# Kernel tuning notes

Hardware: AMD Instinct MI355X
Metric: run time of the kernel (lower is better)

Reference implementation:

```python
import jax, jax.numpy as jnp
import numpy as np

NC = 32          # number of cells
NDIM = 1         # 1D CPAB
NSTEPS = 32      # nstepsolver


def _expm_affine1d(A):
    """Closed-form matrix exponential of [[a, b], [0, 0]] (batched).

    A: [M, 1, 2] -> returns [M, 2, 2] with expm = [[e^a, b*phi(a)], [0, 1]],
    phi(a) = (e^a - 1)/a, with a stable small-a branch.
    """
    a = A[:, 0, 0]
    b = A[:, 0, 1]
    small = jnp.abs(a) < 1e-6
    a_safe = jnp.where(small, 1.0, a)
    phi = jnp.where(small, 1.0 + 0.5 * a, jnp.expm1(a_safe) / a_safe)
    top = jnp.stack([jnp.exp(a), b * phi], axis=-1)            # [M, 2]
    bot = jnp.broadcast_to(jnp.array([0.0, 1.0], dtype=A.dtype), top.shape)
    return jnp.stack([top, bot], axis=-2)                       # [M, 2, 2]


def setup_inputs() -> dict:
    key = jax.random.key(0)
    k1, k2, k3 = jax.random.split(key, 3)
    n_points, n_theta, d = 262144, 8, 30
    points = jax.random.uniform(k1, (NDIM, n_points), dtype=jnp.float32)
    theta = 0.5 * jax.random.normal(k2, (n_theta, d), dtype=jnp.float32)
    basis = 0.3 * jax.random.normal(k3, ((NDIM + 1) * NDIM * NC, d), dtype=jnp.float32)
    return {"points": points, "theta": theta, "basis": basis}


def reference(points, theta, basis):
    n_points = points.shape[1]
    n_theta = theta.shape[0]
    dT = 1.0 / NSTEPS

    # Per-cell affine velocity matrices: Avees [2*nC, n_theta] -> As [n_theta*nC, 1, 2]
    Avees = basis @ theta.T
    As = Avees.T.reshape(n_theta * NC, NDIM, NDIM + 1)
    Trels = _expm_affine1d(dT * As)                               # [n_theta*nC, 2, 2]

    # Repeat points per theta (theta-major flatten order, matching torch code)
    x = jnp.tile(points[0], n_theta)                              # [N]
    pts = jnp.stack([x, jnp.ones_like(x)], axis=-1)               # [N, 2] homogeneous
    batch_idx = NC * jnp.repeat(jnp.arange(n_theta, dtype=jnp.int32), n_points)

    def step(p, _):
        cell = jnp.clip(jnp.floor(p[:, 0] * NC), 0, NC - 1).astype(jnp.int32)
        T = Trels[cell + batch_idx]                               # [N, 2, 2] gather
        return jnp.einsum('nij,nj->ni', T, p), None

    pts, _ = jax.lax.scan(step, pts, None, length=NSTEPS)

    # [N, 1] -> [n_theta, ndim, n_points]
    return pts[:, :NDIM].reshape(n_theta, n_points, NDIM).transpose(0, 2, 1)
```

## Files before the change

kernel.cpp:

```cpp
#include <hip/hip_runtime.h>
#include <math.h>

#define NC 32
#define NSTEPS 32

constexpr int BLOCK = 256;
constexpr int PTS_PER_THREAD = 4;
constexpr int CHUNK = BLOCK * PTS_PER_THREAD;

__global__ void __launch_bounds__(BLOCK)
cpab_kernel(const float* __restrict__ points,
            const float* __restrict__ theta,
            const float* __restrict__ basis,
            float* __restrict__ out,
            int n_points, int d) {
    __shared__ float2 tab[NC];

    const int blocks_per_theta = n_points / CHUNK;
    const int j = blockIdx.x / blocks_per_theta;
    const int tid = threadIdx.x;

    if (tid < NC) {
        const int c = tid;
        const float* __restrict__ th = theta + j * d;
        const float* __restrict__ ba = basis + (2 * c) * d;
        const float* __restrict__ bb = basis + (2 * c + 1) * d;
        float a = 0.0f, b = 0.0f;
#pragma unroll 6
        for (int k = 0; k < d; ++k) {
            float t = th[k];
            a = fmaf(ba[k], t, a);
            b = fmaf(bb[k], t, b);
        }
        const float dT = 1.0f / (float)NSTEPS;
        a *= dT;
        b *= dT;
        float A = expf(a);
        float phi = (fabsf(a) < 1e-6f) ? (1.0f + 0.5f * a) : (expm1f(a) / a);
        tab[c] = make_float2(A, b * phi);
    }
    __syncthreads();

    const int base = (blockIdx.x % blocks_per_theta) * CHUNK + tid * 4;

    float4 v = *(const float4*)(points + base);
    float x[PTS_PER_THREAD] = {v.x, v.y, v.z, v.w};

#pragma unroll
    for (int s = 0; s < NSTEPS; ++s) {
#pragma unroll
        for (int i = 0; i < PTS_PER_THREAD; ++i) {
            float cf = fminf(fmaxf(floorf(x[i] * (float)NC), 0.0f),
                             (float)(NC - 1));
            float2 t = tab[(int)cf];
            x[i] = fmaf(t.x, x[i], t.y);
        }
    }

    float4 o = make_float4(x[0], x[1], x[2], x[3]);
    *(float4*)(out + j * n_points + base) = o;
}

extern "C" void kernel_launch(void* const* d_in, const int* in_sizes, int n_in,
                              void* d_out, int out_size, void* d_ws, size_t ws_size,
                              hipStream_t stream) {
    const float* points = (const float*)d_in[0];
    const float* theta  = (const float*)d_in[1];
    const float* basis  = (const float*)d_in[2];

    int n_points = in_sizes[0];
    int d        = in_sizes[2] / (2 * NC);
    int n_theta  = in_sizes[1] / d;

    int grid = n_theta * (n_points / CHUNK);
    cpab_kernel<<<grid, BLOCK, 0, stream>>>(points, theta, basis,
                                            (float*)d_out, n_points, d);
}
```

Baseline: 74.09 us.

## Precompose 32-step affine maps per fine bin with slow-path fallback

Adds a pre-kernel that, for each theta and each of 8192 fine input bins, composes the 32 cell-wise affine steps into a single affine map. Each bin is flagged pure when both of its endpoints follow the same cell sequence. The main kernel loads this table into shared memory and evaluates each point with one lookup and one FMA. Points in impure bins go to a compacted shared-memory list and are integrated step by step in a scaled coordinate. This removes most of the 32-step serial loop, at the cost of an extra launch, a 64KB shared table per block, and a dependence on workspace memory and on the bin-purity test being exact.

```diff
diff --git a/kernel.cpp b/kernel.cpp
--- a/kernel.cpp
+++ b/kernel.cpp
@@ -3,23 +3,11 @@
 
 #define NC 32
 #define NSTEPS 32
+#define NB 8192
 
-constexpr int BLOCK = 256;
-constexpr int PTS_PER_THREAD = 4;
-constexpr int CHUNK = BLOCK * PTS_PER_THREAD;
-
-__global__ void __launch_bounds__(BLOCK)
-cpab_kernel(const float* __restrict__ points,
-            const float* __restrict__ theta,
-            const float* __restrict__ basis,
-            float* __restrict__ out,
-            int n_points, int d) {
-    __shared__ float2 tab[NC];
-
-    const int blocks_per_theta = n_points / CHUNK;
-    const int j = blockIdx.x / blocks_per_theta;
-    const int tid = threadIdx.x;
-
+__device__ inline void compute_tab(float* tb, const float* __restrict__ theta,
+                                   const float* __restrict__ basis,
+                                   int j, int d, int tid) {
     if (tid < NC) {
         const int c = tid;
         const float* __restrict__ th = theta + j * d;
@@ -37,28 +25,104 @@
         b *= dT;
         float A = expf(a);
         float phi = (fabsf(a) < 1e-6f) ? (1.0f + 0.5f * a) : (expm1f(a) / a);
-        tab[c] = make_float2(A, b * phi);
+        tb[c]      = A;
+        tb[c + NC] = 32.0f * (b * phi);
+    }
+}
+
+__global__ void __launch_bounds__(256)
+compose_kernel(const float* __restrict__ theta,
+               const float* __restrict__ basis,
+               float2* __restrict__ ST, int d) {
+    __shared__ float tb[2 * NC];
+    const int j  = blockIdx.x >> 5;
+    const int i0 = (blockIdx.x & 31) * 256;
+
+    compute_tab(tb, theta, basis, j, d, threadIdx.x);
+    __syncthreads();
+
+    const int i = i0 + threadIdx.x;
+    float zlo = (float)i * 0.00390625f;
+    float zhi = __uint_as_float(
+        __float_as_uint((float)(i + 1) * 0.00390625f) - 1u);
+    double Sd = 1.0, Td = 0.0;
+    bool pure = true;
+#pragma unroll
+    for (int s = 0; s < NSTEPS; ++s) {
+        float flo = fminf(fmaxf(zlo, 0.0f), 31.5f);
+        float fhi = fminf(fmaxf(zhi, 0.0f), 31.5f);
+        int clo = (int)flo, chi = (int)fhi;
+        pure = pure && (clo == chi);
+        float Al = tb[clo], Bl = tb[NC + clo];
+        float Ah = tb[chi], Bh = tb[NC + chi];
+        Sd *= (double)Al;
+        Td = fma((double)Al, Td, (double)Bl);
+        zlo = fmaf(Al, zlo, Bl);
+        zhi = fmaf(Ah, zhi, Bh);
+    }
+    float S = (float)Sd;
+    ST[j * NB + i] = make_float2(pure ? S : -S, (float)(Td * (1.0 / 32.0)));
+}
+
+constexpr int MT     = 512;
+constexpr int MPTS   = 8;
+constexpr int MCHUNK = MT * MPTS;
+
+__global__ void __launch_bounds__(MT)
+main_kernel(const float* __restrict__ points,
+            const float* __restrict__ theta,
+            const float* __restrict__ basis,
+            const float2* __restrict__ ST,
+            float* __restrict__ out,
+            int n_points, int d) {
+    __shared__ float2 st[NB];
+    __shared__ unsigned short ll[MCHUNK];
+    __shared__ float tb[2 * NC];
+    __shared__ unsigned lcnt;
+
+    const int bpt = n_points / MCHUNK;
+    const int j = blockIdx.x / bpt;
+    const int cbase = (blockIdx.x % bpt) * MCHUNK;
+    const int tid = threadIdx.x;
+
+    compute_tab(tb, theta, basis, j, d, tid);
+    {
+        const float4* src = (const float4*)(ST + j * NB);
+        float4* dst = (float4*)st;
+#pragma unroll
+        for (int k = 0; k < NB / 2 / MT; ++k)
+            dst[k * MT + tid] = src[k * MT + tid];
+    }
+    if (tid == 0) lcnt = 0;
+    __syncthreads();
+
+#pragma unroll
+    for (int i = 0; i < MPTS; ++i) {
+        int off = i * MT + tid;
+        float x = points[cbase + off];
+        float f = fminf(fmaxf(x * 8192.0f, 0.0f), 8191.5f);
+        float2 t = st[(int)f];
+        if (t.x > 0.0f) {
+            out[j * n_points + cbase + off] = fmaf(t.x, x, t.y);
+        } else {
+            unsigned s = atomicAdd(&lcnt, 1u);
+            ll[s] = (unsigned short)off;
+        }
     }
     __syncthreads();
 
-    const int base = (blockIdx.x % blocks_per_theta) * CHUNK + tid * 4;
-
-    float4 v = *(const float4*)(points + base);
-    float x[PTS_PER_THREAD] = {v.x, v.y, v.z, v.w};
-
+    unsigned n = lcnt;
+    for (unsigned k = tid; k < n; k += MT) {
+        int off = ll[k];
+        float z = points[cbase + off] * 32.0f;
 #pragma unroll
-    for (int s = 0; s < NSTEPS; ++s) {
-#pragma unroll
-        for (int i = 0; i < PTS_PER_THREAD; ++i) {
-            float cf = fminf(fmaxf(floorf(x[i] * (float)NC), 0.0f),
-                             (float)(NC - 1));
-            float2 t = tab[(int)cf];
-            x[i] = fmaf(t.x, x[i], t.y);
+        for (int s = 0; s < NSTEPS; ++s) {
+            float zc = fminf(fmaxf(z, 0.0f), 31.5f);
+            int c = (int)zc;
+            z = fmaf(tb[c], z, tb[NC + c]);
         }
+        out[j * n_points + cbase + off] = z * 0.03125f;
     }
-
-    float4 o = make_float4(x[0], x[1], x[2], x[3]);
-    *(float4*)(out + j * n_points + base) = o;
 }
 
 extern "C" void kernel_launch(void* const* d_in, const int* in_sizes, int n_in,
@@ -72,7 +136,10 @@
     int d        = in_sizes[2] / (2 * NC);
     int n_theta  = in_sizes[1] / d;
 
-    int grid = n_theta * (n_points / CHUNK);
-    cpab_kernel<<<grid, BLOCK, 0, stream>>>(points, theta, basis,
-                                            (float*)d_out, n_points, d);
+    float2* ST = (float2*)d_ws;
+
+    compose_kernel<<<n_theta * (NB / 256), 256, 0, stream>>>(
+        theta, basis, ST, d);
+    main_kernel<<<n_theta * (n_points / MCHUNK), MT, 0, stream>>>(
+        points, theta, basis, ST, (float*)d_out, n_points, d);
 }
```

Measured after the change: 72.41 us. 2.3% less time.
